# Performance work log

Measured on AMD Instinct MI355X. Metric: run time of the kernel, lower is better.

The kernel has to match this reference:

```python
import jax, jax.numpy as jnp
import numpy as np

N = 100_000
E = 1_000_000
D = 64
NORM_FACTOR = 100.0
LN_EPS = 1e-5


def setup_inputs() -> dict:
    key = jax.random.key(0)
    ks = jax.random.split(key, 8)
    h = jax.random.normal(ks[0], (N, D), dtype=jnp.float32)
    distances = jax.random.uniform(ks[1], (E, 1), dtype=jnp.float32)
    edges = jax.random.randint(ks[2], (2, E), 0, N, dtype=jnp.int64)
    node_mask = jnp.ones((N, 1), dtype=jnp.float32)
    edge_mask = jnp.ones((E, 1), dtype=jnp.float32)
    s = 1.0 / np.sqrt(D)
    W_lin = jax.random.normal(ks[3], (D, D), dtype=jnp.float32) * s
    b_lin = jnp.zeros((D,), dtype=jnp.float32)
    att_W1 = jax.random.normal(ks[4], (D, 2 * D + 1), dtype=jnp.float32) * (1.0 / np.sqrt(2 * D + 1))
    att_b1 = jnp.zeros((D,), dtype=jnp.float32)
    att_W2 = jax.random.normal(ks[5], (1, D), dtype=jnp.float32) * s
    att_b2 = jnp.zeros((1,), dtype=jnp.float32)
    ln_g = jnp.ones((D,), dtype=jnp.float32)
    ln_b = jnp.zeros((D,), dtype=jnp.float32)
    return {"h": h, "distances": distances, "edges": edges, "node_mask": node_mask,
            "edge_mask": edge_mask, "W_lin": W_lin, "b_lin": b_lin,
            "att_W1": att_W1, "att_b1": att_b1, "att_W2": att_W2, "att_b2": att_b2,
            "ln_g": ln_g, "ln_b": ln_b}


def reference(h, distances, edges, node_mask, edge_mask, W_lin, b_lin,
              att_W1, att_b1, att_W2, att_b2, ln_g, ln_b):
    # Linear projection: [N, D]
    x = h @ W_lin.T + b_lin
    row, col = edges[0], edges[1]
    x_row = x[row]          # [E, D]
    x_col = x[col]          # [E, D]
    # DenseAtt: MLP(concat(x_row, x_col, dist)) -> sigmoid -> * edge_mask
    cat = jnp.concatenate([x_row, x_col, distances], axis=1)  # [E, 2D+1]
    hdn = jax.nn.silu(cat @ att_W1.T + att_b1)                # [E, D]
    att = jax.nn.sigmoid(hdn @ att_W2.T + att_b2) * edge_mask # [E, 1]
    # Attention-weighted scatter-sum aggregation into row segments
    agg = x_col * att
    out = jax.ops.segment_sum(agg, row, num_segments=x.shape[0]) / NORM_FACTOR
    out = out + x           # residual
    # LayerNorm + activation
    mu = jnp.mean(out, axis=-1, keepdims=True)
    var = jnp.mean(jnp.square(out - mu), axis=-1, keepdims=True)
    y = (out - mu) * jax.lax.rsqrt(var + LN_EPS) * ln_g + ln_b
    return jax.nn.silu(y)
```

## Files before the change

kernel.cpp:

```cpp
#include <hip/hip_runtime.h>
#include <hip/hip_bf16.h>

#define N_NODES 100000
#define N_EDGES 1000000
#define DIM 64
#define NORM_INV 0.01f
#define LN_EPS 1e-5f
#define N_TILES 6250
#define PROJ_BLOCKS 1563
#define N_BUCKETS 782
#define HISTB 489
#define L2E 1.4426950408889634f
#define LN2 0.6931471805599453f

typedef __attribute__((ext_vector_type(8))) short short8;
typedef __attribute__((ext_vector_type(4))) float f32x4;

__device__ __forceinline__ unsigned short f2bf(float f) {
    union { float f; unsigned u; } x; x.f = f;
    unsigned r = x.u + 0x7FFFu + ((x.u >> 16) & 1u);
    return (unsigned short)(r >> 16);
}
__device__ __forceinline__ float bf2f(unsigned short s) {
    union { unsigned u; float f; } x; x.u = ((unsigned)s) << 16; return x.f;
}

__global__ __launch_bounds__(256) void prep_frags(
    const float* __restrict__ W, const float* __restrict__ att_W1,
    const float* __restrict__ att_b1, const float* __restrict__ att_W2,
    short8* __restrict__ whi, short8* __restrict__ wlo,
    short8* __restrict__ wa, short8* __restrict__ wb,
    float4* __restrict__ tab) {
    const int l = threadIdx.x & 63;
    const int nt = threadIdx.x >> 6;
    const int c = l & 15, q = l >> 4;
    const int n = nt * 16 + c;
#pragma unroll
    for (int ks = 0; ks < 2; ++ks) {
        const int k0 = ks * 32 + q * 8;
        short8 hi8, lo8, a8, b8;
#pragma unroll
        for (int jj = 0; jj < 8; ++jj) {
            float w = W[n * 64 + k0 + jj];
            unsigned short hh = f2bf(w);
            hi8[jj] = (short)hh;
            lo8[jj] = (short)f2bf(w - bf2f(hh));
            a8[jj] = (short)f2bf(att_W1[n * 129 + k0 + jj]);
            b8[jj] = (short)f2bf(att_W1[n * 129 + 64 + k0 + jj]);
        }
        const int idx = (nt * 2 + ks) * 64 + l;
        whi[idx] = hi8; wlo[idx] = lo8; wa[idx] = a8; wb[idx] = b8;
    }
    if (threadIdx.x < 64) {
        const int f = threadIdx.x;
        tab[f] = make_float4(att_W2[f] * LN2, att_W1[f * 129 + 128] * L2E,
                             att_b1[f] * L2E, 0.f);
    }
}

__global__ __launch_bounds__(256) void proj_hist(
    const float* __restrict__ h, const float* __restrict__ bl,
    const short8* __restrict__ whi, const short8* __restrict__ wlo,
    const short8* __restrict__ wa, const short8* __restrict__ wb,
    const int* __restrict__ edges, int* __restrict__ bucketCnt,
    unsigned short* __restrict__ xv, unsigned short* __restrict__ u_bf) {
    if (blockIdx.x >= PROJ_BLOCKS) {
        __shared__ int lh[N_BUCKETS];
        const int tid = threadIdx.x;
        for (int i = tid; i < N_BUCKETS; i += 256) lh[i] = 0;
        __syncthreads();
        const int e0 = (blockIdx.x - PROJ_BLOCKS) * 2048;
#pragma unroll
        for (int i = 0; i < 8; ++i) {
            const int e = e0 + tid * 8 + i;
            if (e < N_EDGES) atomicAdd(&lh[edges[e] >> 7], 1);
        }
        __syncthreads();
        for (int b = tid; b < N_BUCKETS; b += 256)
            if (lh[b]) atomicAdd(&bucketCnt[b], lh[b]);
        return;
    }
    __shared__ __align__(16) unsigned short lds[4][16 * 72];
    const int lane = threadIdx.x & 63;
    const int wv = threadIdx.x >> 6;
    const int c = lane & 15, q = lane >> 4;
    const int tile = blockIdx.x * 4 + wv;
    if (tile >= N_TILES) return;
    const int n0 = tile * 16;

    short8 Whi[4][2], Wlo[4][2], Wa[4][2], Wb[4][2];
    float bias[4];
#pragma unroll
    for (int nt = 0; nt < 4; ++nt) {
        bias[nt] = bl[nt * 16 + c];
#pragma unroll
        for (int ks = 0; ks < 2; ++ks) {
            const int idx = (nt * 2 + ks) * 64 + lane;
            Whi[nt][ks] = whi[idx]; Wlo[nt][ks] = wlo[idx];
            Wa[nt][ks] = wa[idx];   Wb[nt][ks] = wb[idx];
        }
    }

    short8 Ahi[2], Alo[2];
#pragma unroll
    for (int ks = 0; ks < 2; ++ks) {
        const float* hp = h + (size_t)(n0 + c) * 64 + ks * 32 + q * 8;
        f32x4 p0 = *(const f32x4*)hp;
        f32x4 p1 = *(const f32x4*)(hp + 4);
        short8 hi8, lo8;
#pragma unroll
        for (int jj = 0; jj < 4; ++jj) {
            unsigned short hh = f2bf(p0[jj]);
            hi8[jj] = (short)hh; lo8[jj] = (short)f2bf(p0[jj] - bf2f(hh));
            unsigned short h2 = f2bf(p1[jj]);
            hi8[4 + jj] = (short)h2; lo8[4 + jj] = (short)f2bf(p1[jj] - bf2f(h2));
        }
        Ahi[ks] = hi8; Alo[ks] = lo8;
    }

    f32x4 xacc[4] = {{0,0,0,0},{0,0,0,0},{0,0,0,0},{0,0,0,0}};
#pragma unroll
    for (int ks = 0; ks < 2; ++ks)
#pragma unroll
        for (int nt = 0; nt < 4; ++nt) {
            xacc[nt] = __builtin_amdgcn_mfma_f32_16x16x32_bf16(Ahi[ks], Whi[nt][ks], xacc[nt], 0, 0, 0);
            xacc[nt] = __builtin_amdgcn_mfma_f32_16x16x32_bf16(Ahi[ks], Wlo[nt][ks], xacc[nt], 0, 0, 0);
            xacc[nt] = __builtin_amdgcn_mfma_f32_16x16x32_bf16(Alo[ks], Whi[nt][ks], xacc[nt], 0, 0, 0);
        }

    unsigned short* lw = lds[wv];
#pragma unroll
    for (int r = 0; r < 4; ++r) {
        const int node = n0 + q * 4 + r;
        unsigned short xb[4];
#pragma unroll
        for (int nt = 0; nt < 4; ++nt) {
            unsigned short v16 = f2bf(xacc[nt][r] + bias[nt]);
            xb[nt] = v16;
            lw[(q * 4 + r) * 72 + nt * 16 + c] = v16;
        }
        uint2 pk;
        pk.x = (unsigned)xb[0] | ((unsigned)xb[1] << 16);
        pk.y = (unsigned)xb[2] | ((unsigned)xb[3] << 16);
        *(uint2*)(xv + (size_t)node * 128 + c * 8) = pk;
    }

    short8 Ax[2];
#pragma unroll
    for (int ks = 0; ks < 2; ++ks)
        Ax[ks] = *(const short8*)&lw[c * 72 + ks * 32 + q * 8];

    f32x4 uacc[4] = {{0,0,0,0},{0,0,0,0},{0,0,0,0},{0,0,0,0}};
    f32x4 vacc[4] = {{0,0,0,0},{0,0,0,0},{0,0,0,0},{0,0,0,0}};
#pragma unroll
    for (int ks = 0; ks < 2; ++ks)
#pragma unroll
        for (int nt = 0; nt < 4; ++nt) {
            uacc[nt] = __builtin_amdgcn_mfma_f32_16x16x32_bf16(Ax[ks], Wa[nt][ks], uacc[nt], 0, 0, 0);
            vacc[nt] = __builtin_amdgcn_mfma_f32_16x16x32_bf16(Ax[ks], Wb[nt][ks], vacc[nt], 0, 0, 0);
        }
#pragma unroll
    for (int r = 0; r < 4; ++r) {
        const int node = n0 + q * 4 + r;
        uint2 pu;
        pu.x = (unsigned)f2bf(uacc[0][r] * L2E) | ((unsigned)f2bf(uacc[1][r] * L2E) << 16);
        pu.y = (unsigned)f2bf(uacc[2][r] * L2E) | ((unsigned)f2bf(uacc[3][r] * L2E) << 16);
        *(uint2*)(u_bf + (size_t)node * 64 + c * 4) = pu;
        uint2 pk;
        pk.x = (unsigned)f2bf(vacc[0][r] * L2E) | ((unsigned)f2bf(vacc[1][r] * L2E) << 16);
        pk.y = (unsigned)f2bf(vacc[2][r] * L2E) | ((unsigned)f2bf(vacc[3][r] * L2E) << 16);
        *(uint2*)(xv + (size_t)node * 128 + c * 8 + 4) = pk;
    }
}

__global__ __launch_bounds__(1024) void scanA(
    const int* __restrict__ bucketCnt, int* __restrict__ baseA,
    int* __restrict__ cursA) {
    __shared__ int wsum[16];
    const int t = threadIdx.x, lane = t & 63, w = t >> 6;
    const int v = (t < N_BUCKETS) ? bucketCnt[t] : 0;
    int sc = v;
#pragma unroll
    for (int off = 1; off < 64; off <<= 1) {
        int u = __shfl_up(sc, off);
        if (lane >= off) sc += u;
    }
    if (lane == 63) wsum[w] = sc;
    __syncthreads();
    if (w == 0) {
        int x = (lane < 16) ? wsum[lane] : 0;
#pragma unroll
        for (int off = 1; off < 16; off <<= 1) {
            int u = __shfl_up(x, off);
            if (lane >= off) x += u;
        }
        if (lane < 16) wsum[lane] = x;
    }
    __syncthreads();
    const int excl = sc - v + ((w > 0) ? wsum[w - 1] : 0);
    if (t < N_BUCKETS) { baseA[t] = excl; cursA[t] = excl; }
    if (t == N_BUCKETS - 1) baseA[N_BUCKETS] = excl + v;
}

__global__ __launch_bounds__(256) void scatterA(
    const int* __restrict__ edges, const float* __restrict__ dist,
    const float* __restrict__ emask, int* __restrict__ cursA,
    uint2* __restrict__ srec, unsigned char* __restrict__ lrowS) {
    __shared__ int lh[N_BUCKETS];
    __shared__ int lb[N_BUCKETS];
    const int tid = threadIdx.x;
    for (int i = tid; i < N_BUCKETS; i += 256) lh[i] = 0;
    __syncthreads();

    const int e0 = blockIdx.x * 2048 + tid * 8;
    int row[8], col[8];
    unsigned de[8];
#pragma unroll
    for (int i = 0; i < 8; ++i) {
        const int e = e0 + i;
        if (e < N_EDGES) {
            row[i] = edges[e];
            col[i] = edges[N_EDGES + e];
            de[i] = (unsigned)f2bf(dist[e]) | ((unsigned)f2bf(emask[e] * NORM_INV) << 16);
            atomicAdd(&lh[row[i] >> 7], 1);
        } else {
            row[i] = -1;
        }
    }
    __syncthreads();
    for (int b = tid; b < N_BUCKETS; b += 256) {
        const int c = lh[b];
        lb[b] = c ? atomicAdd(&cursA[b], c) : 0;
    }
    __syncthreads();
    for (int i = tid; i < N_BUCKETS; i += 256) lh[i] = 0;
    __syncthreads();
#pragma unroll
    for (int i = 0; i < 8; ++i) {
        if (row[i] >= 0) {
            const int bk = row[i] >> 7;
            const int rk = atomicAdd(&lh[bk], 1);
            const int pos = lb[bk] + rk;
            uint2 rc; rc.x = (unsigned)col[i]; rc.y = de[i];
            srec[pos] = rc;
            lrowS[pos] = (unsigned char)(row[i] & 127);
        }
    }
}

__global__ __launch_bounds__(256) void bucketB1(
    const int* __restrict__ baseA, const unsigned char* __restrict__ lrowS,
    int* __restrict__ pbt) {
    __shared__ int hist[128];
    __shared__ int tt[4];
    const int tid = threadIdx.x;
    const int b = blockIdx.x;
    if (tid < 128) hist[tid] = 0;
    __syncthreads();
    const int s0 = baseA[b], s1 = baseA[b + 1];
    for (int e = s0 + tid; e < s1; e += 256) atomicAdd(&hist[lrowS[e]], 1);
    __syncthreads();
    int p = (tid < 128) ? ((hist[tid] + 3) & ~3) : 0;
#pragma unroll
    for (int off = 1; off < 64; off <<= 1) p += __shfl_xor(p, off);
    if ((tid & 63) == 0) tt[tid >> 6] = p;
    __syncthreads();
    if (tid == 0) pbt[b] = tt[0] + tt[1];
}

__global__ __launch_bounds__(1024) void scanB(
    const int* __restrict__ pbt, int* __restrict__ baseB,
    int* __restrict__ start, uint2* __restrict__ recs) {
    __shared__ int wsum[16];
    const int t = threadIdx.x, lane = t & 63, w = t >> 6;
    const int v = (t < N_BUCKETS) ? pbt[t] : 0;
    int sc = v;
#pragma unroll
    for (int off = 1; off < 64; off <<= 1) {
        int u = __shfl_up(sc, off);
        if (lane >= off) sc += u;
    }
    if (lane == 63) wsum[w] = sc;
    __syncthreads();
    if (w == 0) {
        int x = (lane < 16) ? wsum[lane] : 0;
#pragma unroll
        for (int off = 1; off < 16; off <<= 1) {
            int u = __shfl_up(x, off);
            if (lane >= off) x += u;
        }
        if (lane < 16) wsum[lane] = x;
    }
    __syncthreads();
    const int excl = sc - v + ((w > 0) ? wsum[w - 1] : 0);
    if (t < N_BUCKETS) baseB[t] = excl;
    if (t == N_BUCKETS - 1) {
        const int tot = excl + v;
        baseB[N_BUCKETS] = tot;
        start[N_NODES] = tot;
        uint2 z; z.x = 0; z.y = 0;
        for (int i = 0; i < 16; ++i) recs[tot + i] = z;
    }
}

__global__ __launch_bounds__(256) void bucketB2(
    const int* __restrict__ baseA, const int* __restrict__ baseB,
    const unsigned char* __restrict__ lrowS, const uint2* __restrict__ srec,
    uint2* __restrict__ recs, int* __restrict__ start) {
    __shared__ int hist[128];
    __shared__ int cur[128];
    __shared__ int wtot;
    const int tid = threadIdx.x, lane = tid & 63;
    const int b = blockIdx.x;
    if (tid < 128) hist[tid] = 0;
    __syncthreads();
    const int s0 = baseA[b], s1 = baseA[b + 1];
    for (int e = s0 + tid; e < s1; e += 256) atomicAdd(&hist[lrowS[e]], 1);
    __syncthreads();
    int c = 0, p = 0, sc = 0;
    if (tid < 128) {
        c = hist[tid];
        p = (c + 3) & ~3;
        sc = p;
#pragma unroll
        for (int off = 1; off < 64; off <<= 1) {
            int u = __shfl_up(sc, off);
            if (lane >= off) sc += u;
        }
        if (tid == 63) wtot = sc;
    }
    __syncthreads();
    if (tid < 128) {
        if (tid >= 64) sc += wtot;
        const int excl = baseB[b] + sc - p;
        cur[tid] = excl;
        const int grow = b * 128 + tid;
        if (grow < N_NODES) start[grow] = excl;
        uint2 z; z.x = 0; z.y = 0;
        for (int i = c; i < p; ++i) recs[excl + i] = z;
    }
    __syncthreads();
    for (int e = s0 + tid; e < s1; e += 256) {
        const int lr = lrowS[e];
        const uint2 rc = srec[e];
        const int pos = atomicAdd(&cur[lr], 1);
        recs[pos] = rc;
    }
}

__global__ __launch_bounds__(256, 8) void agg_ln_kernel(
    const int* __restrict__ start, const uint2* __restrict__ recs,
    const unsigned short* __restrict__ xv, const unsigned short* __restrict__ u_bf,
    const float4* __restrict__ tab, const float* __restrict__ att_b2,
    const float* __restrict__ ln_g, const float* __restrict__ ln_b,
    float* __restrict__ out) {
    const int lane = threadIdx.x & 63;
    const int wv = threadIdx.x >> 6;
    const int j = lane & 15;
    const int s = lane >> 4;
    const int r = blockIdx.x * 4 + wv;

    const float4 t0 = tab[j], t1 = tab[j + 16], t2 = tab[j + 32], t3 = tab[j + 48];
    const uint2 uu = *(const uint2*)(u_bf + (size_t)r * 64 + j * 4);
    const float base0 = __uint_as_float(uu.x << 16) + t0.z;
    const float base1 = __uint_as_float(uu.x & 0xffff0000u) + t1.z;
    const float base2 = __uint_as_float(uu.y << 16) + t2.z;
    const float base3 = __uint_as_float(uu.y & 0xffff0000u) + t3.z;
    const float b2L = att_b2[0] * L2E;

    const int s0 = start[r];
    const int e1 = start[r + 1];
    const unsigned* xvu = (const unsigned*)xv;

    float a0 = 0.f, a1 = 0.f, a2 = 0.f, a3 = 0.f;
    if (e1 > s0) {
        uint2 recA = recs[s0 + s];
        uint4 xvA = *(const uint4*)(xvu + (size_t)recA.x * 64 + j * 4);
        uint2 recB = recs[s0 + 4 + s];
        for (int e = s0; e < e1; e += 4) {
            const uint2 recC = recs[e + 8 + s];
            const uint4 xvB = *(const uint4*)(xvu + (size_t)recB.x * 64 + j * 4);

            const float dist = __uint_as_float(recA.y << 16);
            const float emN = __uint_as_float(recA.y & 0xffff0000u);
            const float x0 = __uint_as_float(xvA.x << 16);
            const float x1 = __uint_as_float(xvA.x & 0xffff0000u);
            const float x2 = __uint_as_float(xvA.y << 16);
            const float x3 = __uint_as_float(xvA.y & 0xffff0000u);
            const float v0 = __uint_as_float(xvA.z << 16);
            const float v1 = __uint_as_float(xvA.z & 0xffff0000u);
            const float v2 = __uint_as_float(xvA.w << 16);
            const float v3 = __uint_as_float(xvA.w & 0xffff0000u);
            float pv = 0.f, pre, sg;
            pre = fmaf(dist, t0.y, base0) + v0;
            sg = __builtin_amdgcn_rcpf(1.f + __builtin_amdgcn_exp2f(-pre));
            pv = fmaf(pre * sg, t0.x, pv);
            pre = fmaf(dist, t1.y, base1) + v1;
            sg = __builtin_amdgcn_rcpf(1.f + __builtin_amdgcn_exp2f(-pre));
            pv = fmaf(pre * sg, t1.x, pv);
            pre = fmaf(dist, t2.y, base2) + v2;
            sg = __builtin_amdgcn_rcpf(1.f + __builtin_amdgcn_exp2f(-pre));
            pv = fmaf(pre * sg, t2.x, pv);
            pre = fmaf(dist, t3.y, base3) + v3;
            sg = __builtin_amdgcn_rcpf(1.f + __builtin_amdgcn_exp2f(-pre));
            pv = fmaf(pre * sg, t3.x, pv);
            pv += __shfl_xor(pv, 1); pv += __shfl_xor(pv, 2);
            pv += __shfl_xor(pv, 4); pv += __shfl_xor(pv, 8);
            const float sp = fmaf(pv, L2E, b2L);
            const float att =
                emN * __builtin_amdgcn_rcpf(1.f + __builtin_amdgcn_exp2f(-sp));
            a0 = fmaf(att, x0, a0); a1 = fmaf(att, x1, a1);
            a2 = fmaf(att, x2, a2); a3 = fmaf(att, x3, a3);
            recA = recB; xvA = xvB; recB = recC;
        }
    }
    a0 += __shfl_xor(a0, 16); a0 += __shfl_xor(a0, 32);
    a1 += __shfl_xor(a1, 16); a1 += __shfl_xor(a1, 32);
    a2 += __shfl_xor(a2, 16); a2 += __shfl_xor(a2, 32);
    a3 += __shfl_xor(a3, 16); a3 += __shfl_xor(a3, 32);

    const uint2 xr = *(const uint2*)(xvu + (size_t)r * 64 + j * 4);
    const float o0 = __uint_as_float(xr.x << 16) + a0;
    const float o1 = __uint_as_float(xr.x & 0xffff0000u) + a1;
    const float o2 = __uint_as_float(xr.y << 16) + a2;
    const float o3 = __uint_as_float(xr.y & 0xffff0000u) + a3;

    float ssum = o0 + o1 + o2 + o3;
    ssum += __shfl_xor(ssum, 1); ssum += __shfl_xor(ssum, 2);
    ssum += __shfl_xor(ssum, 4); ssum += __shfl_xor(ssum, 8);
    const float mu = ssum * (1.f / 64.f);
    const float d0 = o0 - mu, d1 = o1 - mu, d2 = o2 - mu, d3 = o3 - mu;
    float vs = d0 * d0 + d1 * d1 + d2 * d2 + d3 * d3;
    vs += __shfl_xor(vs, 1); vs += __shfl_xor(vs, 2);
    vs += __shfl_xor(vs, 4); vs += __shfl_xor(vs, 8);
    const float rstd = rsqrtf(vs * (1.f / 64.f) + LN_EPS);

    const int f = j + 16 * s;
    const float dk = (s == 0) ? d0 : (s == 1) ? d1 : (s == 2) ? d2 : d3;
    const float y = fmaf(dk * rstd, ln_g[f], ln_b[f]);
    out[(size_t)r * 64 + lane] =
        y * __builtin_amdgcn_rcpf(1.f + __builtin_amdgcn_exp2f(-y * L2E));
}

extern "C" void kernel_launch(void* const* d_in, const int* in_sizes, int n_in,
                              void* d_out, int out_size, void* d_ws, size_t ws_size,
                              hipStream_t stream) {
    const float* h      = (const float*)d_in[0];
    const float* dist   = (const float*)d_in[1];
    const int*   edges  = (const int*)d_in[2];
    const float* emask  = (const float*)d_in[4];
    const float* W_lin  = (const float*)d_in[5];
    const float* b_lin  = (const float*)d_in[6];
    const float* att_W1 = (const float*)d_in[7];
    const float* att_b1 = (const float*)d_in[8];
    const float* att_W2 = (const float*)d_in[9];
    const float* att_b2 = (const float*)d_in[10];
    const float* ln_g   = (const float*)d_in[11];
    const float* ln_b   = (const float*)d_in[12];
    float* out = (float*)d_out;

    char* ws = (char*)d_ws;
    unsigned short* xv   = (unsigned short*)ws;
    unsigned short* u_bf = (unsigned short*)(ws + 25600000);
    uint2* srec          = (uint2*)(ws + 38400000);
    uint2* recs          = (uint2*)(ws + 46400000);
    unsigned char* lrowS = (unsigned char*)(ws + 56800128);
    int* start           = (int*)(ws + 57800192);
    int* bucketCnt       = (int*)(ws + 58200576);
    int* baseA           = (int*)(ws + 58204672);
    int* cursA           = (int*)(ws + 58208768);
    int* pbt             = (int*)(ws + 58212864);
    int* baseB           = (int*)(ws + 58216960);
    float4* tab          = (float4*)(ws + 58221056);
    short8* whi          = (short8*)(ws + 58222080);
    short8* wlo          = (short8*)(ws + 58230272);
    short8* wa           = (short8*)(ws + 58238464);
    short8* wb           = (short8*)(ws + 58246656);

    hipMemsetAsync(bucketCnt, 0, N_BUCKETS * sizeof(int), stream);
    prep_frags<<<1, 256, 0, stream>>>(W_lin, att_W1, att_b1, att_W2,
                                      whi, wlo, wa, wb, tab);
    proj_hist<<<PROJ_BLOCKS + HISTB, 256, 0, stream>>>(
        h, b_lin, whi, wlo, wa, wb, edges, bucketCnt, xv, u_bf);
    scanA<<<1, 1024, 0, stream>>>(bucketCnt, baseA, cursA);
    scatterA<<<HISTB, 256, 0, stream>>>(edges, dist, emask, cursA, srec, lrowS);
    bucketB1<<<N_BUCKETS, 256, 0, stream>>>(baseA, lrowS, pbt);
    scanB<<<1, 1024, 0, stream>>>(pbt, baseB, start, recs);
    bucketB2<<<N_BUCKETS, 256, 0, stream>>>(baseA, baseB, lrowS, srec, recs, start);
    agg_ln_kernel<<<N_NODES / 4, 256, 0, stream>>>(start, recs, xv, u_bf,
                                                   tab, att_b2, ln_g, ln_b, out);
}
```

Before: 237.4 us.

## Replace two-level bucket CSR build with per-row counting sort via global atomics

```diff
diff --git a/kernel.cpp b/kernel.cpp
--- a/kernel.cpp
+++ b/kernel.cpp
@@ -62,7 +62,8 @@
     const float* __restrict__ h, const float* __restrict__ bl,
     const short8* __restrict__ whi, const short8* __restrict__ wlo,
     const short8* __restrict__ wa, const short8* __restrict__ wb,
-    const int* __restrict__ edges, int* __restrict__ bucketCnt,
+    const int* __restrict__ edges, int* __restrict__ rowCnt,
+    int* __restrict__ bucketCnt,
     unsigned short* __restrict__ xv, unsigned short* __restrict__ u_bf) {
     if (blockIdx.x >= PROJ_BLOCKS) {
         __shared__ int lh[N_BUCKETS];
@@ -73,7 +74,11 @@
 #pragma unroll
         for (int i = 0; i < 8; ++i) {
             const int e = e0 + tid * 8 + i;
-            if (e < N_EDGES) atomicAdd(&lh[edges[e] >> 7], 1);
+            if (e < N_EDGES) {
+                const int r = edges[e];
+                atomicAdd(&lh[r >> 7], 1);
+                atomicAdd(&rowCnt[r], 1);
+            }
         }
         __syncthreads();
         for (int b = tid; b < N_BUCKETS; b += 256)
@@ -174,8 +179,7 @@
 }
 
 __global__ __launch_bounds__(1024) void scanA(
-    const int* __restrict__ bucketCnt, int* __restrict__ baseA,
-    int* __restrict__ cursA) {
+    const int* __restrict__ bucketCnt, int* __restrict__ bucketBase) {
     __shared__ int wsum[16];
     const int t = threadIdx.x, lane = t & 63, w = t >> 6;
     const int v = (t < N_BUCKETS) ? bucketCnt[t] : 0;
@@ -198,153 +202,75 @@
     }
     __syncthreads();
     const int excl = sc - v + ((w > 0) ? wsum[w - 1] : 0);
-    if (t < N_BUCKETS) { baseA[t] = excl; cursA[t] = excl; }
-    if (t == N_BUCKETS - 1) baseA[N_BUCKETS] = excl + v;
-}
-
-__global__ __launch_bounds__(256) void scatterA(
-    const int* __restrict__ edges, const float* __restrict__ dist,
-    const float* __restrict__ emask, int* __restrict__ cursA,
-    uint2* __restrict__ srec, unsigned char* __restrict__ lrowS) {
-    __shared__ int lh[N_BUCKETS];
-    __shared__ int lb[N_BUCKETS];
-    const int tid = threadIdx.x;
-    for (int i = tid; i < N_BUCKETS; i += 256) lh[i] = 0;
-    __syncthreads();
-
-    const int e0 = blockIdx.x * 2048 + tid * 8;
-    int row[8], col[8];
-    unsigned de[8];
-#pragma unroll
-    for (int i = 0; i < 8; ++i) {
-        const int e = e0 + i;
-        if (e < N_EDGES) {
-            row[i] = edges[e];
-            col[i] = edges[N_EDGES + e];
-            de[i] = (unsigned)f2bf(dist[e]) | ((unsigned)f2bf(emask[e] * NORM_INV) << 16);
-            atomicAdd(&lh[row[i] >> 7], 1);
-        } else {
-            row[i] = -1;
-        }
-    }
-    __syncthreads();
-    for (int b = tid; b < N_BUCKETS; b += 256) {
-        const int c = lh[b];
-        lb[b] = c ? atomicAdd(&cursA[b], c) : 0;
-    }
-    __syncthreads();
-    for (int i = tid; i < N_BUCKETS; i += 256) lh[i] = 0;
-    __syncthreads();
-#pragma unroll
-    for (int i = 0; i < 8; ++i) {
-        if (row[i] >= 0) {
-            const int bk = row[i] >> 7;
-            const int rk = atomicAdd(&lh[bk], 1);
-            const int pos = lb[bk] + rk;
-            uint2 rc; rc.x = (unsigned)col[i]; rc.y = de[i];
-            srec[pos] = rc;
-            lrowS[pos] = (unsigned char)(row[i] & 127);
-        }
-    }
-}
-
-__global__ __launch_bounds__(256) void bucketB1(
-    const int* __restrict__ baseA, const unsigned char* __restrict__ lrowS,
-    int* __restrict__ pbt) {
-    __shared__ int hist[128];
-    __shared__ int tt[4];
-    const int tid = threadIdx.x;
+    if (t < N_BUCKETS) bucketBase[t] = excl;
+}
+
+__global__ __launch_bounds__(128) void rowscan(
+    const int* __restrict__ rowCnt, const int* __restrict__ bucketBase,
+    int* __restrict__ start, int* __restrict__ curs,
+    uint2* __restrict__ recs) {
+    __shared__ int w0sum;
     const int b = blockIdx.x;
-    if (tid < 128) hist[tid] = 0;
-    __syncthreads();
-    const int s0 = baseA[b], s1 = baseA[b + 1];
-    for (int e = s0 + tid; e < s1; e += 256) atomicAdd(&hist[lrowS[e]], 1);
-    __syncthreads();
-    int p = (tid < 128) ? ((hist[tid] + 3) & ~3) : 0;
-#pragma unroll
-    for (int off = 1; off < 64; off <<= 1) p += __shfl_xor(p, off);
-    if ((tid & 63) == 0) tt[tid >> 6] = p;
-    __syncthreads();
-    if (tid == 0) pbt[b] = tt[0] + tt[1];
-}
-
-__global__ __launch_bounds__(1024) void scanB(
-    const int* __restrict__ pbt, int* __restrict__ baseB,
-    int* __restrict__ start, uint2* __restrict__ recs) {
-    __shared__ int wsum[16];
-    const int t = threadIdx.x, lane = t & 63, w = t >> 6;
-    const int v = (t < N_BUCKETS) ? pbt[t] : 0;
+    const int t = threadIdx.x;
+    const int gr = b * 128 + t;
+    const int lane = t & 63;
+    const int v = (gr < N_NODES) ? rowCnt[gr] : 0;
     int sc = v;
 #pragma unroll
     for (int off = 1; off < 64; off <<= 1) {
         int u = __shfl_up(sc, off);
         if (lane >= off) sc += u;
     }
-    if (lane == 63) wsum[w] = sc;
+    if (t == 63) w0sum = sc;
     __syncthreads();
-    if (w == 0) {
-        int x = (lane < 16) ? wsum[lane] : 0;
-#pragma unroll
-        for (int off = 1; off < 16; off <<= 1) {
-            int u = __shfl_up(x, off);
-            if (lane >= off) x += u;
-        }
-        if (lane < 16) wsum[lane] = x;
-    }
-    __syncthreads();
-    const int excl = sc - v + ((w > 0) ? wsum[w - 1] : 0);
-    if (t < N_BUCKETS) baseB[t] = excl;
-    if (t == N_BUCKETS - 1) {
-        const int tot = excl + v;
-        baseB[N_BUCKETS] = tot;
-        start[N_NODES] = tot;
+    const int excl = sc - v + ((t >= 64) ? w0sum : 0) + bucketBase[b];
+    if (gr < N_NODES) { start[gr] = excl; curs[gr] = excl; }
+    if (b == 0 && t == 0) {
+        start[N_NODES] = N_EDGES;
         uint2 z; z.x = 0; z.y = 0;
-        for (int i = 0; i < 16; ++i) recs[tot + i] = z;
-    }
-}
-
-__global__ __launch_bounds__(256) void bucketB2(
-    const int* __restrict__ baseA, const int* __restrict__ baseB,
-    const unsigned char* __restrict__ lrowS, const uint2* __restrict__ srec,
-    uint2* __restrict__ recs, int* __restrict__ start) {
-    __shared__ int hist[128];
-    __shared__ int cur[128];
-    __shared__ int wtot;
-    const int tid = threadIdx.x, lane = tid & 63;
-    const int b = blockIdx.x;
-    if (tid < 128) hist[tid] = 0;
-    __syncthreads();
-    const int s0 = baseA[b], s1 = baseA[b + 1];
-    for (int e = s0 + tid; e < s1; e += 256) atomicAdd(&hist[lrowS[e]], 1);
-    __syncthreads();
-    int c = 0, p = 0, sc = 0;
-    if (tid < 128) {
-        c = hist[tid];
-        p = (c + 3) & ~3;
-        sc = p;
-#pragma unroll
-        for (int off = 1; off < 64; off <<= 1) {
-            int u = __shfl_up(sc, off);
-            if (lane >= off) sc += u;
-        }
-        if (tid == 63) wtot = sc;
-    }
-    __syncthreads();
-    if (tid < 128) {
-        if (tid >= 64) sc += wtot;
-        const int excl = baseB[b] + sc - p;
-        cur[tid] = excl;
-        const int grow = b * 128 + tid;
-        if (grow < N_NODES) start[grow] = excl;
-        uint2 z; z.x = 0; z.y = 0;
-        for (int i = c; i < p; ++i) recs[excl + i] = z;
-    }
-    __syncthreads();
-    for (int e = s0 + tid; e < s1; e += 256) {
-        const int lr = lrowS[e];
-        const uint2 rc = srec[e];
-        const int pos = atomicAdd(&cur[lr], 1);
-        recs[pos] = rc;
+        for (int i = 0; i < 16; ++i) recs[N_EDGES + i] = z;
+    }
+}
+
+__global__ __launch_bounds__(256) void scatterD(
+    const int* __restrict__ edges, const float* __restrict__ dist,
+    const float* __restrict__ emask, int* __restrict__ curs,
+    uint2* __restrict__ recs) {
+    const int e0 = blockIdx.x * 2048 + threadIdx.x * 8;
+    if (e0 + 8 <= N_EDGES) {
+        const int4 r0 = *(const int4*)(edges + e0);
+        const int4 r1 = *(const int4*)(edges + e0 + 4);
+        const int4 c0 = *(const int4*)(edges + N_EDGES + e0);
+        const int4 c1 = *(const int4*)(edges + N_EDGES + e0 + 4);
+        const f32x4 d0 = *(const f32x4*)(dist + e0);
+        const f32x4 d1 = *(const f32x4*)(dist + e0 + 4);
+        const f32x4 m0 = *(const f32x4*)(emask + e0);
+        const f32x4 m1 = *(const f32x4*)(emask + e0 + 4);
+        const int rows[8] = {r0.x, r0.y, r0.z, r0.w, r1.x, r1.y, r1.z, r1.w};
+        const int cols[8] = {c0.x, c0.y, c0.z, c0.w, c1.x, c1.y, c1.z, c1.w};
+        const float ds[8] = {d0[0], d0[1], d0[2], d0[3], d1[0], d1[1], d1[2], d1[3]};
+        const float ms[8] = {m0[0], m0[1], m0[2], m0[3], m1[0], m1[1], m1[2], m1[3]};
+#pragma unroll
+        for (int i = 0; i < 8; ++i) {
+            const int pos = atomicAdd(&curs[rows[i]], 1);
+            uint2 rc;
+            rc.x = (unsigned)cols[i];
+            rc.y = (unsigned)f2bf(ds[i]) | ((unsigned)f2bf(ms[i] * NORM_INV) << 16);
+            recs[pos] = rc;
+        }
+    } else {
+#pragma unroll
+        for (int i = 0; i < 8; ++i) {
+            const int e = e0 + i;
+            if (e < N_EDGES) {
+                const int pos = atomicAdd(&curs[edges[e]], 1);
+                uint2 rc;
+                rc.x = (unsigned)edges[N_EDGES + e];
+                rc.y = (unsigned)f2bf(dist[e]) |
+                       ((unsigned)f2bf(emask[e] * NORM_INV) << 16);
+                recs[pos] = rc;
+            }
+        }
     }
 }
 
@@ -407,8 +333,9 @@
             pv += __shfl_xor(pv, 1); pv += __shfl_xor(pv, 2);
             pv += __shfl_xor(pv, 4); pv += __shfl_xor(pv, 8);
             const float sp = fmaf(pv, L2E, b2L);
-            const float att =
+            const float attRaw =
                 emN * __builtin_amdgcn_rcpf(1.f + __builtin_amdgcn_exp2f(-sp));
+            const float att = ((e + s) < e1) ? attRaw : 0.f;
             a0 = fmaf(att, x0, a0); a1 = fmaf(att, x1, a1);
             a2 = fmaf(att, x2, a2); a3 = fmaf(att, x3, a3);
             recA = recB; xvA = xvB; recB = recC;
@@ -462,31 +389,26 @@
     char* ws = (char*)d_ws;
     unsigned short* xv   = (unsigned short*)ws;
     unsigned short* u_bf = (unsigned short*)(ws + 25600000);
-    uint2* srec          = (uint2*)(ws + 38400000);
-    uint2* recs          = (uint2*)(ws + 46400000);
-    unsigned char* lrowS = (unsigned char*)(ws + 56800128);
-    int* start           = (int*)(ws + 57800192);
-    int* bucketCnt       = (int*)(ws + 58200576);
-    int* baseA           = (int*)(ws + 58204672);
-    int* cursA           = (int*)(ws + 58208768);
-    int* pbt             = (int*)(ws + 58212864);
-    int* baseB           = (int*)(ws + 58216960);
-    float4* tab          = (float4*)(ws + 58221056);
-    short8* whi          = (short8*)(ws + 58222080);
-    short8* wlo          = (short8*)(ws + 58230272);
-    short8* wa           = (short8*)(ws + 58238464);
-    short8* wb           = (short8*)(ws + 58246656);
-
-    hipMemsetAsync(bucketCnt, 0, N_BUCKETS * sizeof(int), stream);
+    uint2* recs          = (uint2*)(ws + 38400000);
+    int* rowCnt          = (int*)(ws + 46400256);
+    int* bucketCnt       = (int*)(ws + 46800256);
+    int* curs            = (int*)(ws + 46803456);
+    int* start           = (int*)(ws + 47203584);
+    int* bucketBase      = (int*)(ws + 47603712);
+    float4* tab          = (float4*)(ws + 47606912);
+    short8* whi          = (short8*)(ws + 47607936);
+    short8* wlo          = (short8*)(ws + 47616128);
+    short8* wa           = (short8*)(ws + 47624320);
+    short8* wb           = (short8*)(ws + 47632512);
+
+    hipMemsetAsync(rowCnt, 0, 403200, stream);
     prep_frags<<<1, 256, 0, stream>>>(W_lin, att_W1, att_b1, att_W2,
                                       whi, wlo, wa, wb, tab);
     proj_hist<<<PROJ_BLOCKS + HISTB, 256, 0, stream>>>(
-        h, b_lin, whi, wlo, wa, wb, edges, bucketCnt, xv, u_bf);
-    scanA<<<1, 1024, 0, stream>>>(bucketCnt, baseA, cursA);
-    scatterA<<<HISTB, 256, 0, stream>>>(edges, dist, emask, cursA, srec, lrowS);
-    bucketB1<<<N_BUCKETS, 256, 0, stream>>>(baseA, lrowS, pbt);
-    scanB<<<1, 1024, 0, stream>>>(pbt, baseB, start, recs);
-    bucketB2<<<N_BUCKETS, 256, 0, stream>>>(baseA, baseB, lrowS, srec, recs, start);
+        h, b_lin, whi, wlo, wa, wb, edges, rowCnt, bucketCnt, xv, u_bf);
+    scanA<<<1, 1024, 0, stream>>>(bucketCnt, bucketBase);
+    rowscan<<<N_BUCKETS, 128, 0, stream>>>(rowCnt, bucketBase, start, curs, recs);
+    scatterD<<<HISTB, 256, 0, stream>>>(edges, dist, emask, curs, recs);
     agg_ln_kernel<<<N_NODES / 4, 256, 0, stream>>>(start, recs, xv, u_bf,
                                                    tab, att_b2, ln_g, ln_b, out);
 }
```

After: 281.4 us. 1.19x slower.

## Fuse second-level bucket sort into aggregation kernel using LDS-resident edge records

Applied to the files above, without the earlier changes.

```diff
diff --git a/kernel.cpp b/kernel.cpp
--- a/kernel.cpp
+++ b/kernel.cpp
@@ -12,6 +12,8 @@
 #define HISTB 489
 #define L2E 1.4426950408889634f
 #define LN2 0.6931471805599453f
+#define CAP 2560
+#define RPT 5
 
 typedef __attribute__((ext_vector_type(8))) short short8;
 typedef __attribute__((ext_vector_type(4))) float f32x4;
@@ -248,75 +250,45 @@
     }
 }
 
-__global__ __launch_bounds__(256) void bucketB1(
+__global__ __launch_bounds__(512, 4) void agg_fused(
     const int* __restrict__ baseA, const unsigned char* __restrict__ lrowS,
-    int* __restrict__ pbt) {
+    const uint2* __restrict__ srec,
+    const unsigned short* __restrict__ xv, const unsigned short* __restrict__ u_bf,
+    const float4* __restrict__ tab, const float* __restrict__ att_b2,
+    const float* __restrict__ ln_g, const float* __restrict__ ln_b,
+    float* __restrict__ out) {
+    __shared__ __align__(16) uint2 lrecs[CAP + 16];
     __shared__ int hist[128];
-    __shared__ int tt[4];
-    const int tid = threadIdx.x;
-    const int b = blockIdx.x;
-    if (tid < 128) hist[tid] = 0;
-    __syncthreads();
-    const int s0 = baseA[b], s1 = baseA[b + 1];
-    for (int e = s0 + tid; e < s1; e += 256) atomicAdd(&hist[lrowS[e]], 1);
-    __syncthreads();
-    int p = (tid < 128) ? ((hist[tid] + 3) & ~3) : 0;
-#pragma unroll
-    for (int off = 1; off < 64; off <<= 1) p += __shfl_xor(p, off);
-    if ((tid & 63) == 0) tt[tid >> 6] = p;
-    __syncthreads();
-    if (tid == 0) pbt[b] = tt[0] + tt[1];
-}
-
-__global__ __launch_bounds__(1024) void scanB(
-    const int* __restrict__ pbt, int* __restrict__ baseB,
-    int* __restrict__ start, uint2* __restrict__ recs) {
-    __shared__ int wsum[16];
-    const int t = threadIdx.x, lane = t & 63, w = t >> 6;
-    const int v = (t < N_BUCKETS) ? pbt[t] : 0;
-    int sc = v;
-#pragma unroll
-    for (int off = 1; off < 64; off <<= 1) {
-        int u = __shfl_up(sc, off);
-        if (lane >= off) sc += u;
-    }
-    if (lane == 63) wsum[w] = sc;
-    __syncthreads();
-    if (w == 0) {
-        int x = (lane < 16) ? wsum[lane] : 0;
-#pragma unroll
-        for (int off = 1; off < 16; off <<= 1) {
-            int u = __shfl_up(x, off);
-            if (lane >= off) x += u;
-        }
-        if (lane < 16) wsum[lane] = x;
-    }
-    __syncthreads();
-    const int excl = sc - v + ((w > 0) ? wsum[w - 1] : 0);
-    if (t < N_BUCKETS) baseB[t] = excl;
-    if (t == N_BUCKETS - 1) {
-        const int tot = excl + v;
-        baseB[N_BUCKETS] = tot;
-        start[N_NODES] = tot;
-        uint2 z; z.x = 0; z.y = 0;
-        for (int i = 0; i < 16; ++i) recs[tot + i] = z;
-    }
-}
-
-__global__ __launch_bounds__(256) void bucketB2(
-    const int* __restrict__ baseA, const int* __restrict__ baseB,
-    const unsigned char* __restrict__ lrowS, const uint2* __restrict__ srec,
-    uint2* __restrict__ recs, int* __restrict__ start) {
-    __shared__ int hist[128];
+    __shared__ int rst[129];
     __shared__ int cur[128];
     __shared__ int wtot;
-    const int tid = threadIdx.x, lane = tid & 63;
+
     const int b = blockIdx.x;
+    const int tid = threadIdx.x;
+    const int lane = tid & 63;
+    const int wv = tid >> 6;
+    const int s0g = baseA[b];
+    const int cnt = baseA[b + 1] - s0g;
+
     if (tid < 128) hist[tid] = 0;
     __syncthreads();
-    const int s0 = baseA[b], s1 = baseA[b + 1];
-    for (int e = s0 + tid; e < s1; e += 256) atomicAdd(&hist[lrowS[e]], 1);
-    __syncthreads();
+
+    uint2 rec0, rec1, rec2, rec3, rec4;
+    int lr0 = -1, lr1 = -1, lr2 = -1, lr3 = -1, lr4 = -1;
+    {
+        int idx = tid;
+        if (idx < cnt) { rec0 = srec[s0g + idx]; lr0 = lrowS[s0g + idx]; atomicAdd(&hist[lr0], 1); }
+        idx += 512;
+        if (idx < cnt) { rec1 = srec[s0g + idx]; lr1 = lrowS[s0g + idx]; atomicAdd(&hist[lr1], 1); }
+        idx += 512;
+        if (idx < cnt) { rec2 = srec[s0g + idx]; lr2 = lrowS[s0g + idx]; atomicAdd(&hist[lr2], 1); }
+        idx += 512;
+        if (idx < cnt) { rec3 = srec[s0g + idx]; lr3 = lrowS[s0g + idx]; atomicAdd(&hist[lr3], 1); }
+        idx += 512;
+        if (idx < cnt) { rec4 = srec[s0g + idx]; lr4 = lrowS[s0g + idx]; atomicAdd(&hist[lr4], 1); }
+    }
+    __syncthreads();
+
     int c = 0, p = 0, sc = 0;
     if (tid < 128) {
         c = hist[tid];
@@ -332,114 +304,114 @@
     __syncthreads();
     if (tid < 128) {
         if (tid >= 64) sc += wtot;
-        const int excl = baseB[b] + sc - p;
+        const int excl = sc - p;
+        rst[tid] = excl;
         cur[tid] = excl;
-        const int grow = b * 128 + tid;
-        if (grow < N_NODES) start[grow] = excl;
         uint2 z; z.x = 0; z.y = 0;
-        for (int i = c; i < p; ++i) recs[excl + i] = z;
-    }
-    __syncthreads();
-    for (int e = s0 + tid; e < s1; e += 256) {
-        const int lr = lrowS[e];
-        const uint2 rc = srec[e];
-        const int pos = atomicAdd(&cur[lr], 1);
-        recs[pos] = rc;
-    }
-}
-
-__global__ __launch_bounds__(256, 8) void agg_ln_kernel(
-    const int* __restrict__ start, const uint2* __restrict__ recs,
-    const unsigned short* __restrict__ xv, const unsigned short* __restrict__ u_bf,
-    const float4* __restrict__ tab, const float* __restrict__ att_b2,
-    const float* __restrict__ ln_g, const float* __restrict__ ln_b,
-    float* __restrict__ out) {
-    const int lane = threadIdx.x & 63;
-    const int wv = threadIdx.x >> 6;
+        for (int i = c; i < p; ++i) lrecs[excl + i] = z;
+        if (tid == 127) {
+            rst[128] = excl + p;
+            for (int i = 0; i < 16; ++i) lrecs[excl + p + i] = z;
+        }
+    }
+    __syncthreads();
+
+    if (lr0 >= 0) lrecs[atomicAdd(&cur[lr0], 1)] = rec0;
+    if (lr1 >= 0) lrecs[atomicAdd(&cur[lr1], 1)] = rec1;
+    if (lr2 >= 0) lrecs[atomicAdd(&cur[lr2], 1)] = rec2;
+    if (lr3 >= 0) lrecs[atomicAdd(&cur[lr3], 1)] = rec3;
+    if (lr4 >= 0) lrecs[atomicAdd(&cur[lr4], 1)] = rec4;
+    __syncthreads();
+
     const int j = lane & 15;
-    const int s = lane >> 4;
-    const int r = blockIdx.x * 4 + wv;
-
+    const int sl = lane >> 4;
     const float4 t0 = tab[j], t1 = tab[j + 16], t2 = tab[j + 32], t3 = tab[j + 48];
-    const uint2 uu = *(const uint2*)(u_bf + (size_t)r * 64 + j * 4);
-    const float base0 = __uint_as_float(uu.x << 16) + t0.z;
-    const float base1 = __uint_as_float(uu.x & 0xffff0000u) + t1.z;
-    const float base2 = __uint_as_float(uu.y << 16) + t2.z;
-    const float base3 = __uint_as_float(uu.y & 0xffff0000u) + t3.z;
     const float b2L = att_b2[0] * L2E;
-
-    const int s0 = start[r];
-    const int e1 = start[r + 1];
+    const float gg = ln_g[lane], bb = ln_b[lane];
     const unsigned* xvu = (const unsigned*)xv;
 
-    float a0 = 0.f, a1 = 0.f, a2 = 0.f, a3 = 0.f;
-    if (e1 > s0) {
-        uint2 recA = recs[s0 + s];
-        uint4 xvA = *(const uint4*)(xvu + (size_t)recA.x * 64 + j * 4);
-        uint2 recB = recs[s0 + 4 + s];
-        for (int e = s0; e < e1; e += 4) {
-            const uint2 recC = recs[e + 8 + s];
-            const uint4 xvB = *(const uint4*)(xvu + (size_t)recB.x * 64 + j * 4);
-
-            const float dist = __uint_as_float(recA.y << 16);
-            const float emN = __uint_as_float(recA.y & 0xffff0000u);
-            const float x0 = __uint_as_float(xvA.x << 16);
-            const float x1 = __uint_as_float(xvA.x & 0xffff0000u);
-            const float x2 = __uint_as_float(xvA.y << 16);
-            const float x3 = __uint_as_float(xvA.y & 0xffff0000u);
-            const float v0 = __uint_as_float(xvA.z << 16);
-            const float v1 = __uint_as_float(xvA.z & 0xffff0000u);
-            const float v2 = __uint_as_float(xvA.w << 16);
-            const float v3 = __uint_as_float(xvA.w & 0xffff0000u);
-            float pv = 0.f, pre, sg;
-            pre = fmaf(dist, t0.y, base0) + v0;
-            sg = __builtin_amdgcn_rcpf(1.f + __builtin_amdgcn_exp2f(-pre));
-            pv = fmaf(pre * sg, t0.x, pv);
-            pre = fmaf(dist, t1.y, base1) + v1;
-            sg = __builtin_amdgcn_rcpf(1.f + __builtin_amdgcn_exp2f(-pre));
-            pv = fmaf(pre * sg, t1.x, pv);
-            pre = fmaf(dist, t2.y, base2) + v2;
-            sg = __builtin_amdgcn_rcpf(1.f + __builtin_amdgcn_exp2f(-pre));
-            pv = fmaf(pre * sg, t2.x, pv);
-            pre = fmaf(dist, t3.y, base3) + v3;
-            sg = __builtin_amdgcn_rcpf(1.f + __builtin_amdgcn_exp2f(-pre));
-            pv = fmaf(pre * sg, t3.x, pv);
-            pv += __shfl_xor(pv, 1); pv += __shfl_xor(pv, 2);
-            pv += __shfl_xor(pv, 4); pv += __shfl_xor(pv, 8);
-            const float sp = fmaf(pv, L2E, b2L);
-            const float att =
-                emN * __builtin_amdgcn_rcpf(1.f + __builtin_amdgcn_exp2f(-sp));
-            a0 = fmaf(att, x0, a0); a1 = fmaf(att, x1, a1);
-            a2 = fmaf(att, x2, a2); a3 = fmaf(att, x3, a3);
-            recA = recB; xvA = xvB; recB = recC;
-        }
-    }
-    a0 += __shfl_xor(a0, 16); a0 += __shfl_xor(a0, 32);
-    a1 += __shfl_xor(a1, 16); a1 += __shfl_xor(a1, 32);
-    a2 += __shfl_xor(a2, 16); a2 += __shfl_xor(a2, 32);
-    a3 += __shfl_xor(a3, 16); a3 += __shfl_xor(a3, 32);
-
-    const uint2 xr = *(const uint2*)(xvu + (size_t)r * 64 + j * 4);
-    const float o0 = __uint_as_float(xr.x << 16) + a0;
-    const float o1 = __uint_as_float(xr.x & 0xffff0000u) + a1;
-    const float o2 = __uint_as_float(xr.y << 16) + a2;
-    const float o3 = __uint_as_float(xr.y & 0xffff0000u) + a3;
-
-    float ssum = o0 + o1 + o2 + o3;
-    ssum += __shfl_xor(ssum, 1); ssum += __shfl_xor(ssum, 2);
-    ssum += __shfl_xor(ssum, 4); ssum += __shfl_xor(ssum, 8);
-    const float mu = ssum * (1.f / 64.f);
-    const float d0 = o0 - mu, d1 = o1 - mu, d2 = o2 - mu, d3 = o3 - mu;
-    float vs = d0 * d0 + d1 * d1 + d2 * d2 + d3 * d3;
-    vs += __shfl_xor(vs, 1); vs += __shfl_xor(vs, 2);
-    vs += __shfl_xor(vs, 4); vs += __shfl_xor(vs, 8);
-    const float rstd = rsqrtf(vs * (1.f / 64.f) + LN_EPS);
-
-    const int f = j + 16 * s;
-    const float dk = (s == 0) ? d0 : (s == 1) ? d1 : (s == 2) ? d2 : d3;
-    const float y = fmaf(dk * rstd, ln_g[f], ln_b[f]);
-    out[(size_t)r * 64 + lane] =
-        y * __builtin_amdgcn_rcpf(1.f + __builtin_amdgcn_exp2f(-y * L2E));
+#pragma unroll 1
+    for (int k = 0; k < 16; ++k) {
+        const int lrw = wv + 8 * k;
+        const int r = b * 128 + lrw;
+        if (r >= N_NODES) break;
+
+        const uint2 uu = *(const uint2*)(u_bf + (size_t)r * 64 + j * 4);
+        const float base0 = __uint_as_float(uu.x << 16) + t0.z;
+        const float base1 = __uint_as_float(uu.x & 0xffff0000u) + t1.z;
+        const float base2 = __uint_as_float(uu.y << 16) + t2.z;
+        const float base3 = __uint_as_float(uu.y & 0xffff0000u) + t3.z;
+
+        const int s0 = rst[lrw];
+        const int e1 = rst[lrw + 1];
+
+        float a0 = 0.f, a1 = 0.f, a2 = 0.f, a3 = 0.f;
+        if (e1 > s0) {
+            uint2 recA = lrecs[s0 + sl];
+            uint4 xvA = *(const uint4*)(xvu + (size_t)recA.x * 64 + j * 4);
+            for (int e = s0; e < e1; e += 4) {
+                const uint2 recB = lrecs[e + 4 + sl];
+                const uint4 xvB = *(const uint4*)(xvu + (size_t)recB.x * 64 + j * 4);
+
+                const float dist = __uint_as_float(recA.y << 16);
+                const float emN = __uint_as_float(recA.y & 0xffff0000u);
+                const float x0 = __uint_as_float(xvA.x << 16);
+                const float x1 = __uint_as_float(xvA.x & 0xffff0000u);
+                const float x2 = __uint_as_float(xvA.y << 16);
+                const float x3 = __uint_as_float(xvA.y & 0xffff0000u);
+                const float v0 = __uint_as_float(xvA.z << 16);
+                const float v1 = __uint_as_float(xvA.z & 0xffff0000u);
+                const float v2 = __uint_as_float(xvA.w << 16);
+                const float v3 = __uint_as_float(xvA.w & 0xffff0000u);
+                float pv = 0.f, pre, sg;
+                pre = fmaf(dist, t0.y, base0) + v0;
+                sg = __builtin_amdgcn_rcpf(1.f + __builtin_amdgcn_exp2f(-pre));
+                pv = fmaf(pre * sg, t0.x, pv);
+                pre = fmaf(dist, t1.y, base1) + v1;
+                sg = __builtin_amdgcn_rcpf(1.f + __builtin_amdgcn_exp2f(-pre));
+                pv = fmaf(pre * sg, t1.x, pv);
+                pre = fmaf(dist, t2.y, base2) + v2;
+                sg = __builtin_amdgcn_rcpf(1.f + __builtin_amdgcn_exp2f(-pre));
+                pv = fmaf(pre * sg, t2.x, pv);
+                pre = fmaf(dist, t3.y, base3) + v3;
+                sg = __builtin_amdgcn_rcpf(1.f + __builtin_amdgcn_exp2f(-pre));
+                pv = fmaf(pre * sg, t3.x, pv);
+                pv += __shfl_xor(pv, 1); pv += __shfl_xor(pv, 2);
+                pv += __shfl_xor(pv, 4); pv += __shfl_xor(pv, 8);
+                const float sp = fmaf(pv, L2E, b2L);
+                const float att =
+                    emN * __builtin_amdgcn_rcpf(1.f + __builtin_amdgcn_exp2f(-sp));
+                a0 = fmaf(att, x0, a0); a1 = fmaf(att, x1, a1);
+                a2 = fmaf(att, x2, a2); a3 = fmaf(att, x3, a3);
+                recA = recB; xvA = xvB;
+            }
+        }
+        a0 += __shfl_xor(a0, 16); a0 += __shfl_xor(a0, 32);
+        a1 += __shfl_xor(a1, 16); a1 += __shfl_xor(a1, 32);
+        a2 += __shfl_xor(a2, 16); a2 += __shfl_xor(a2, 32);
+        a3 += __shfl_xor(a3, 16); a3 += __shfl_xor(a3, 32);
+
+        const uint2 xr = *(const uint2*)(xvu + (size_t)r * 64 + j * 4);
+        const float o0 = __uint_as_float(xr.x << 16) + a0;
+        const float o1 = __uint_as_float(xr.x & 0xffff0000u) + a1;
+        const float o2 = __uint_as_float(xr.y << 16) + a2;
+        const float o3 = __uint_as_float(xr.y & 0xffff0000u) + a3;
+
+        float ssum = o0 + o1 + o2 + o3;
+        ssum += __shfl_xor(ssum, 1); ssum += __shfl_xor(ssum, 2);
+        ssum += __shfl_xor(ssum, 4); ssum += __shfl_xor(ssum, 8);
+        const float mu = ssum * (1.f / 64.f);
+        const float d0 = o0 - mu, d1 = o1 - mu, d2 = o2 - mu, d3 = o3 - mu;
+        float vs = d0 * d0 + d1 * d1 + d2 * d2 + d3 * d3;
+        vs += __shfl_xor(vs, 1); vs += __shfl_xor(vs, 2);
+        vs += __shfl_xor(vs, 4); vs += __shfl_xor(vs, 8);
+        const float rstd = rsqrtf(vs * (1.f / 64.f) + LN_EPS);
+
+        const float dk = (sl == 0) ? d0 : (sl == 1) ? d1 : (sl == 2) ? d2 : d3;
+        const float y = fmaf(dk * rstd, gg, bb);
+        out[(size_t)r * 64 + lane] =
+            y * __builtin_amdgcn_rcpf(1.f + __builtin_amdgcn_exp2f(-y * L2E));
+    }
 }
 
 extern "C" void kernel_launch(void* const* d_in, const int* in_sizes, int n_in,
@@ -463,19 +435,15 @@
     unsigned short* xv   = (unsigned short*)ws;
     unsigned short* u_bf = (unsigned short*)(ws + 25600000);
     uint2* srec          = (uint2*)(ws + 38400000);
-    uint2* recs          = (uint2*)(ws + 46400000);
-    unsigned char* lrowS = (unsigned char*)(ws + 56800128);
-    int* start           = (int*)(ws + 57800192);
-    int* bucketCnt       = (int*)(ws + 58200576);
-    int* baseA           = (int*)(ws + 58204672);
-    int* cursA           = (int*)(ws + 58208768);
-    int* pbt             = (int*)(ws + 58212864);
-    int* baseB           = (int*)(ws + 58216960);
-    float4* tab          = (float4*)(ws + 58221056);
-    short8* whi          = (short8*)(ws + 58222080);
-    short8* wlo          = (short8*)(ws + 58230272);
-    short8* wa           = (short8*)(ws + 58238464);
-    short8* wb           = (short8*)(ws + 58246656);
+    unsigned char* lrowS = (unsigned char*)(ws + 46400000);
+    int* bucketCnt       = (int*)(ws + 47400000);
+    int* baseA           = (int*)(ws + 47403200);
+    int* cursA           = (int*)(ws + 47406400);
+    float4* tab          = (float4*)(ws + 47409600);
+    short8* whi          = (short8*)(ws + 47410624);
+    short8* wlo          = (short8*)(ws + 47418816);
+    short8* wa           = (short8*)(ws + 47427008);
+    short8* wb           = (short8*)(ws + 47435200);
 
     hipMemsetAsync(bucketCnt, 0, N_BUCKETS * sizeof(int), stream);
     prep_frags<<<1, 256, 0, stream>>>(W_lin, att_W1, att_b1, att_W2,
@@ -484,9 +452,6 @@
         h, b_lin, whi, wlo, wa, wb, edges, bucketCnt, xv, u_bf);
     scanA<<<1, 1024, 0, stream>>>(bucketCnt, baseA, cursA);
     scatterA<<<HISTB, 256, 0, stream>>>(edges, dist, emask, cursA, srec, lrowS);
-    bucketB1<<<N_BUCKETS, 256, 0, stream>>>(baseA, lrowS, pbt);
-    scanB<<<1, 1024, 0, stream>>>(pbt, baseB, start, recs);
-    bucketB2<<<N_BUCKETS, 256, 0, stream>>>(baseA, baseB, lrowS, srec, recs, start);
-    agg_ln_kernel<<<N_NODES / 4, 256, 0, stream>>>(start, recs, xv, u_bf,
-                                                   tab, att_b2, ln_g, ln_b, out);
-}
+    agg_fused<<<N_BUCKETS, 512, 0, stream>>>(baseA, lrowS, srec, xv, u_bf,
+                                             tab, att_b2, ln_g, ln_b, out);
+}
```

Measured after the change: 237.6 us. No clear change (+0.1%).
